# Kernel optimization log

Measured on AMD Instinct MI355X. Metric: run time of the kernel, lower is better.

The kernel has to match this reference:

```python
import jax, jax.numpy as jnp
import numpy as np

HID = 128
N_NODES = 50000
N_EDGES = 800000
N_GRAPHS = 64
N_LAYERS = 2
BN_EPS = 1e-5


def setup_inputs() -> dict:
    key = jax.random.key(0)
    ks = jax.random.split(key, 12)
    x_idx = jax.random.randint(ks[0], (N_NODES,), 0, 19)
    edge_index = jax.random.randint(ks[1], (2, N_EDGES), 0, N_NODES)
    edge_attr = jax.random.randint(ks[2], (N_EDGES,), 0, 4)
    batch = jnp.sort(jax.random.randint(ks[3], (N_NODES,), 0, N_GRAPHS))
    s = 1.0 / np.sqrt(HID)
    node_emb = jax.random.normal(ks[4], (19, HID), jnp.float32)
    edge_emb = jax.random.normal(ks[5], (4, HID), jnp.float32)
    # stacked per-layer GINE MLP params: Linear->ReLU->Linear->ReLU->BN
    W1 = jax.random.uniform(ks[6], (N_LAYERS, HID, HID), jnp.float32, -s, s)
    b1 = jnp.zeros((N_LAYERS, HID), jnp.float32)
    W2 = jax.random.uniform(ks[7], (N_LAYERS, HID, HID), jnp.float32, -s, s)
    b2 = jnp.zeros((N_LAYERS, HID), jnp.float32)
    bn_g = jnp.ones((N_LAYERS, HID), jnp.float32)
    bn_b = jnp.zeros((N_LAYERS, HID), jnp.float32)
    return {"x_idx": x_idx, "edge_index": edge_index, "edge_attr": edge_attr,
            "batch": batch, "node_emb": node_emb, "edge_emb": edge_emb,
            "W1": W1, "b1": b1, "W2": W2, "b2": b2, "bn_g": bn_g, "bn_b": bn_b}


def _gine_layer(x, e_feat, src, dst, W1, b1, W2, b2, g, beta):
    # GINEConv (eps=0): nn(x + sum_{j->i} relu(x_j + e_ji))
    msg = jax.nn.relu(x[src] + e_feat)                       # [E, H] gather
    aggr = jax.ops.segment_sum(msg, dst, num_segments=x.shape[0])  # scatter-add
    h = x + aggr
    h = jax.nn.relu(h @ W1 + b1)
    h = jax.nn.relu(h @ W2 + b2)
    mu = h.mean(0)
    var = h.var(0)
    return g * (h - mu) * jax.lax.rsqrt(var + BN_EPS) + beta  # training-mode BN


def reference(x_idx, edge_index, edge_attr, batch, node_emb, edge_emb,
              W1, b1, W2, b2, bn_g, bn_b):
    x = node_emb[x_idx]                 # [N, H]
    e_feat = edge_emb[edge_attr]        # [E, H] (encoded once, shared by layers)
    src, dst = edge_index[0], edge_index[1]
    for l in range(N_LAYERS):
        x = _gine_layer(x, e_feat, src, dst, W1[l], b1[l], W2[l], b2[l], bn_g[l], bn_b[l])
    pooled = jax.ops.segment_sum(x, batch, num_segments=N_GRAPHS)  # global_add_pool
    return pooled
```

## Files before the change

kernel.cpp:

```cpp
#include <hip/hip_runtime.h>
#include <hip/hip_bf16.h>

#define HID 128
#define NNODES 50000
#define NEDGES 800000
#define NGRAPHS 64
#define BN_EPS 1e-5f
#define CAP 64

typedef __attribute__((ext_vector_type(8))) short short8;
typedef __attribute__((ext_vector_type(4))) float f32x4;

static __device__ __forceinline__ unsigned short f2bf(float v) {
  __hip_bfloat16 b = __float2bfloat16(v);
  return *reinterpret_cast<unsigned short*>(&b);
}
static __device__ __forceinline__ float bf2f(unsigned short u) {
  return __uint_as_float(((unsigned)u) << 16);
}
static __device__ __forceinline__ float lo16f(unsigned u) {
  return __uint_as_float(u << 16);
}
static __device__ __forceinline__ float hi16f(unsigned u) {
  return __uint_as_float(u & 0xFFFF0000u);
}

static __device__ __forceinline__ unsigned packhl(float v) {
  unsigned short h = f2bf(v);
  unsigned short l = f2bf(v - bf2f(h));
  return (unsigned)h | ((unsigned)l << 16);
}
static __device__ __forceinline__ float upk(unsigned p) {
  return __uint_as_float(p << 16) + __uint_as_float(p & 0xFFFF0000u);
}
static __device__ __forceinline__ void unpack8(uint4 wa, uint4 wb,
                                               short8& hi, short8& lo) {
  union U { unsigned u[4]; short8 s; };
  U H, L;
  unsigned w[8] = {wa.x, wa.y, wa.z, wa.w, wb.x, wb.y, wb.z, wb.w};
  #pragma unroll
  for (int t = 0; t < 4; t++) {
    unsigned a = w[2 * t], b = w[2 * t + 1];
    H.u[t] = (a & 0xFFFFu) | (b << 16);
    L.u[t] = (a >> 16) | (b & 0xFFFF0000u);
  }
  hi = H.s; lo = L.s;
}

__global__ __launch_bounds__(256) void prep_kernel(
    const int* __restrict__ x_idx, const float* __restrict__ node_emb,
    const int* __restrict__ eidx, const int* __restrict__ eattr,
    int* __restrict__ cnt, int* __restrict__ eout,
    const float* __restrict__ W1, const float* __restrict__ W2,
    unsigned short* __restrict__ Wpk, unsigned* __restrict__ msgTg,
    unsigned* __restrict__ typeT, const float* __restrict__ edge_emb) {
  int i = blockIdx.x * 256 + threadIdx.x;
  int stride = gridDim.x * 256;
  for (int e = i; e < NEDGES; e += stride) {
    int s = eidx[e];
    int d = eidx[NEDGES + e];
    int ty = x_idx[s];
    int pos = atomicAdd(&cnt[d], 1);
    if (pos < CAP)
      eout[((size_t)d << 6) + pos] = s | (eattr[e] << 16) | (ty << 18);
  }
  for (int idx = i; idx < 76 * 64; idx += stride) {
    int combo = idx >> 6, c2 = (idx & 63) << 1;
    int ty = combo >> 2, at = combo & 3;
    float a0 = fmaxf(node_emb[ty * HID + c2] + edge_emb[at * HID + c2], 0.f);
    float a1 = fmaxf(node_emb[ty * HID + c2 + 1] + edge_emb[at * HID + c2 + 1], 0.f);
    msgTg[idx] = (unsigned)f2bf(a0) | ((unsigned)f2bf(a1) << 16);
  }
  for (int idx = i; idx < 19 * 64; idx += stride) {
    int ty = idx >> 6, c2 = (idx & 63) << 1;
    typeT[idx] = (unsigned)f2bf(node_emb[ty * HID + c2]) |
                 ((unsigned)f2bf(node_emb[ty * HID + c2 + 1]) << 16);
  }
  for (int idx = i; idx < 65536; idx += stride) {
    int j = idx & 7;
    int l = (idx >> 3) & 63;
    int q = (idx >> 9) & 3;
    int t = (idx >> 11) & 7;
    int m = idx >> 14;
    int k = ((l >> 4) << 3) + j + (q << 5);
    int n = (t << 4) + (l & 15);
    int layer = m >> 1;
    const float* W = (m & 1) ? W2 : W1;
    float w = W[(size_t)layer * HID * HID + k * HID + n];
    unsigned short h = f2bf(w);
    Wpk[idx] = h;
    Wpk[idx + 65536] = f2bf(w - bf2f(h));
  }
}

#define NT 32
#define LDAF 132
#define GRID_GINE ((NNODES + NT - 1) / NT)

template <bool L0>
__global__ __launch_bounds__(512, 8) void gine_mlp_kernel(
    const unsigned short* __restrict__ in_bf,
    const int* __restrict__ xidx,
    const float* __restrict__ instats,
    const float* __restrict__ gam, const float* __restrict__ bet,
    const int* __restrict__ cnt, const int* __restrict__ eout,
    const unsigned* __restrict__ msgTg, const float* __restrict__ edge_emb,
    const short8* __restrict__ Wh, const short8* __restrict__ Wl,
    const float* __restrict__ b1, const float* __restrict__ b2,
    unsigned short* __restrict__ out_bf, float* __restrict__ stats,
    const int* __restrict__ batch, float* __restrict__ gpool) {
  extern __shared__ __align__(16) char smem[];
  unsigned* hAp = (unsigned*)smem;
  float* sheL = (float*)(smem + NT * LDAF * 4);
  float* red = (float*)(smem + NT * LDAF * 4);

  const int tid = threadIdx.x;
  const int lane = tid & 63;
  const int wave = tid >> 6;
  const int base = blockIdx.x * NT;

  float scl_lo = 1.0f, scl_hi = 1.0f, sh_lo = 0.0f, sh_hi = 0.0f;

  if constexpr (!L0) {
    if (tid < 4 * HID) {
      int c = tid & 127;
      float mu = instats[c] * (1.0f / NNODES);
      float var = instats[HID + c] * (1.0f / NNODES) - mu * mu;
      float s = gam[c] * rsqrtf(var + BN_EPS);
      float shc = bet[c] - mu * s;
      sheL[tid] = shc + edge_emb[tid];
    }
    {
      int c0 = lane << 1;
      float mu0 = instats[c0] * (1.0f / NNODES);
      float var0 = instats[HID + c0] * (1.0f / NNODES) - mu0 * mu0;
      scl_lo = gam[c0] * rsqrtf(var0 + BN_EPS);
      sh_lo = bet[c0] - mu0 * scl_lo;
      float mu1 = instats[c0 + 1] * (1.0f / NNODES);
      float var1 = instats[HID + c0 + 1] * (1.0f / NNODES) - mu1 * mu1;
      scl_hi = gam[c0 + 1] * rsqrtf(var1 + BN_EPS);
      sh_hi = bet[c0 + 1] - mu1 * scl_hi;
    }
    __syncthreads();
  }

  {
    const unsigned* in4 = (const unsigned*)in_bf;
    int node0 = base + wave * 4;
    float acc0[4], acc1[4];
    #pragma unroll
    for (int i = 0; i < 4; i++) { acc0[i] = 0.0f; acc1[i] = 0.0f; }

    int dg4[4], epw4[4];
    unsigned sv4[4];
    #pragma unroll
    for (int i = 0; i < 4; i++) {
      int node = node0 + i;
      bool v = node < NNODES;
      dg4[i] = v ? __builtin_amdgcn_readfirstlane(min(cnt[node], CAP)) : 0;
      epw4[i] = v ? eout[(node << 6) + lane] : 0;
      int srow;
      if constexpr (L0)
        srow = v ? __builtin_amdgcn_readfirstlane(xidx[node]) : 0;
      else
        srow = node;
      sv4[i] = v ? in4[(srow << 6) + lane] : 0u;
    }

#define GL_ISSUE(SB, X, A)                                      \
    {                                                           \
      _Pragma("unroll")                                         \
      for (int jj = 0; jj < 8; jj++) {                          \
        if ((SB) + jj < dg) {                                   \
          int w = __builtin_amdgcn_readlane(epw, (SB) + jj);    \
          A[jj] = (w >> 16) & 3;                                \
          X[jj] = in4[((w & 0xFFFF) << 6) + lane];              \
        }                                                       \
      }                                                         \
    }
#define GL_CONS(SB, X, A)                                       \
    {                                                           \
      _Pragma("unroll")                                         \
      for (int jj = 0; jj < 8; jj++) {                          \
        if ((SB) + jj < dg) {                                   \
          float2 e2 = *(const float2*)&sheL[(A[jj] << 7) + (lane << 1)]; \
          acc0[i] += fmaxf(fmaf(lo16f(X[jj]), scl_lo, e2.x), 0.0f); \
          acc1[i] += fmaxf(fmaf(hi16f(X[jj]), scl_hi, e2.y), 0.0f); \
        }                                                       \
      }                                                         \
    }
#define GT_ISSUE(SB, M)                                         \
    {                                                           \
      _Pragma("unroll")                                         \
      for (int jj = 0; jj < 8; jj++) {                          \
        if ((SB) + jj < dg) {                                   \
          int w = __builtin_amdgcn_readlane(epw, (SB) + jj);    \
          M[jj] = msgTg[(((w >> 16) & 127) << 6) + lane];       \
        }                                                       \
      }                                                         \
    }
#define GT_CONS(SB, M)                                          \
    {                                                           \
      _Pragma("unroll")                                         \
      for (int jj = 0; jj < 8; jj++) {                          \
        if ((SB) + jj < dg) {                                   \
          acc0[i] += lo16f(M[jj]);                              \
          acc1[i] += hi16f(M[jj]);                              \
        }                                                       \
      }                                                         \
    }

    #pragma unroll
    for (int i = 0; i < 4; i++) {
      int node = node0 + i;
      if (node >= NNODES) continue;
      int dg = dg4[i];
      int epw = epw4[i];
      if constexpr (L0) {
        acc0[i] = lo16f(sv4[i]);
        acc1[i] = hi16f(sv4[i]);
      } else {
        acc0[i] = fmaf(lo16f(sv4[i]), scl_lo, sh_lo);
        acc1[i] = fmaf(hi16f(sv4[i]), scl_hi, sh_hi);
      }
      if (dg > 0) {
        if constexpr (L0) {
          unsigned M0[8], M1[8];
          GT_ISSUE(0, M0);
          int s = 0;
          for (;;) {
            if (s * 8 + 8 < dg) GT_ISSUE(s * 8 + 8, M1);
            GT_CONS(s * 8, M0);
            s++;
            if (s * 8 >= dg) break;
            if (s * 8 + 8 < dg) GT_ISSUE(s * 8 + 8, M0);
            GT_CONS(s * 8, M1);
            s++;
            if (s * 8 >= dg) break;
          }
        } else {
          unsigned X0[8], X1[8];
          int A0[8], A1[8];
          GL_ISSUE(0, X0, A0);
          int s = 0;
          for (;;) {
            if (s * 8 + 8 < dg) GL_ISSUE(s * 8 + 8, X1, A1);
            GL_CONS(s * 8, X0, A0);
            s++;
            if (s * 8 >= dg) break;
            if (s * 8 + 8 < dg) GL_ISSUE(s * 8 + 8, X0, A0);
            GL_CONS(s * 8, X1, A1);
            s++;
            if (s * 8 >= dg) break;
          }
        }
      }
    }
#undef GL_ISSUE
#undef GL_CONS
#undef GT_ISSUE
#undef GT_CONS

    #pragma unroll
    for (int i = 0; i < 4; i++) {
      int nrow = wave * 4 + i;
      hAp[nrow * LDAF + (lane << 1)] = packhl(acc0[i]);
      hAp[nrow * LDAF + (lane << 1) + 1] = packhl(acc1[i]);
    }
  }
  __syncthreads();

  const int col = lane & 15;
  const int quad = lane >> 4;
  const int rbase = quad * 4;
  const int ch0 = wave * 16 + col;
  const int aoff = quad * 8;

  {
    f32x4 a0 = {0.f, 0.f, 0.f, 0.f}, a1 = a0;
    #pragma unroll
    for (int q = 0; q < 4; q++) {
      int f0 = wave * 256 + q * 64 + lane;
      short8 b0h = Wh[f0], b0l = Wl[f0];
      const unsigned* r0 = &hAp[col * LDAF + q * 32 + aoff];
      const unsigned* r1 = &hAp[(16 + col) * LDAF + q * 32 + aoff];
      short8 a0h, a0l, a1h, a1l;
      unpack8(*(const uint4*)r0, *(const uint4*)(r0 + 4), a0h, a0l);
      unpack8(*(const uint4*)r1, *(const uint4*)(r1 + 4), a1h, a1l);
      a0 = __builtin_amdgcn_mfma_f32_16x16x32_bf16(a0h, b0h, a0, 0, 0, 0);
      a0 = __builtin_amdgcn_mfma_f32_16x16x32_bf16(a0l, b0h, a0, 0, 0, 0);
      a0 = __builtin_amdgcn_mfma_f32_16x16x32_bf16(a0h, b0l, a0, 0, 0, 0);
      a1 = __builtin_amdgcn_mfma_f32_16x16x32_bf16(a1h, b0h, a1, 0, 0, 0);
      a1 = __builtin_amdgcn_mfma_f32_16x16x32_bf16(a1l, b0h, a1, 0, 0, 0);
      a1 = __builtin_amdgcn_mfma_f32_16x16x32_bf16(a1h, b0l, a1, 0, 0, 0);
    }
    __syncthreads();
    float bb0 = b1[ch0];
    #pragma unroll
    for (int r = 0; r < 4; r++) {
      hAp[(rbase + r) * LDAF + ch0] = packhl(fmaxf(a0[r] + bb0, 0.0f));
      hAp[(16 + rbase + r) * LDAF + ch0] = packhl(fmaxf(a1[r] + bb0, 0.0f));
    }
  }
  __syncthreads();

  {
    f32x4 a0 = {0.f, 0.f, 0.f, 0.f}, a1 = a0;
    #pragma unroll
    for (int q = 0; q < 4; q++) {
      int f0 = 2048 + wave * 256 + q * 64 + lane;
      short8 b0h = Wh[f0], b0l = Wl[f0];
      const unsigned* r0 = &hAp[col * LDAF + q * 32 + aoff];
      const unsigned* r1 = &hAp[(16 + col) * LDAF + q * 32 + aoff];
      short8 a0h, a0l, a1h, a1l;
      unpack8(*(const uint4*)r0, *(const uint4*)(r0 + 4), a0h, a0l);
      unpack8(*(const uint4*)r1, *(const uint4*)(r1 + 4), a1h, a1l);
      a0 = __builtin_amdgcn_mfma_f32_16x16x32_bf16(a0h, b0h, a0, 0, 0, 0);
      a0 = __builtin_amdgcn_mfma_f32_16x16x32_bf16(a0l, b0h, a0, 0, 0, 0);
      a0 = __builtin_amdgcn_mfma_f32_16x16x32_bf16(a0h, b0l, a0, 0, 0, 0);
      a1 = __builtin_amdgcn_mfma_f32_16x16x32_bf16(a1h, b0h, a1, 0, 0, 0);
      a1 = __builtin_amdgcn_mfma_f32_16x16x32_bf16(a1l, b0h, a1, 0, 0, 0);
      a1 = __builtin_amdgcn_mfma_f32_16x16x32_bf16(a1h, b0l, a1, 0, 0, 0);
    }
    __syncthreads();
    float bb0 = b2[ch0];
    #pragma unroll
    for (int r = 0; r < 4; r++) {
      hAp[(rbase + r) * LDAF + ch0] = packhl(fmaxf(a0[r] + bb0, 0.0f));
      hAp[(16 + rbase + r) * LDAF + ch0] = packhl(fmaxf(a1[r] + bb0, 0.0f));
    }
  }
  __syncthreads();

  float lsum = 0.0f, lsq = 0.0f;
  if (tid < 256) {
    const int c = tid & 127;
    const int yy = tid >> 7;
    if (out_bf) {
      #pragma unroll 4
      for (int i = 0; i < 16; i++) {
        int n = yy * 16 + i;
        int node = base + n;
        if (node < NNODES) {
          unsigned p = hAp[n * LDAF + c];
          out_bf[node * HID + c] = (unsigned short)(p & 0xFFFF);
          float v = upk(p);
          lsum += v;
          lsq += v * v;
        }
      }
    } else {
      int curg = -1;
      float pacc = 0.0f;
      for (int i = 0; i < 16; i++) {
        int n = yy * 16 + i;
        int node = base + n;
        if (node < NNODES) {
          float v = upk(hAp[n * LDAF + c]);
          lsum += v;
          lsq += v * v;
          int bg = batch[node];
          if (bg != curg) {
            if (curg >= 0) unsafeAtomicAdd(&gpool[curg * HID + c], pacc);
            curg = bg;
            pacc = 0.0f;
          }
          pacc += v;
        }
      }
      if (curg >= 0) unsafeAtomicAdd(&gpool[curg * HID + c], pacc);
    }
    if (tid >= 128) {
      red[tid - 128] = lsum;
      red[tid] = lsq;
    }
  }
  __syncthreads();
  if (tid < 128) {
    lsum += red[tid];
    lsq += red[128 + tid];
    unsafeAtomicAdd(&stats[tid], lsum);
    unsafeAtomicAdd(&stats[HID + tid], lsq);
  }
}

__device__ __forceinline__ int lbound(const int* __restrict__ arr, int n,
                                      int key) {
  int lo = 0, hi = n;
  while (lo < hi) {
    int mid = (lo + hi) >> 1;
    if (arr[mid] < key) lo = mid + 1; else hi = mid;
  }
  return lo;
}

__global__ __launch_bounds__(128) void finish_kernel(
    const float* __restrict__ gpool, const float* __restrict__ stats,
    const float* __restrict__ gam, const float* __restrict__ bet,
    const int* __restrict__ batch, float* __restrict__ out) {
  __shared__ int cnt_s;
  int g = blockIdx.x, c = threadIdx.x;
  if (c == 0)
    cnt_s = lbound(batch, NNODES, g + 1) - lbound(batch, NNODES, g);
  __syncthreads();
  float mu = stats[c] * (1.0f / NNODES);
  float var = stats[HID + c] * (1.0f / NNODES) - mu * mu;
  float scl = gam[c] * rsqrtf(var + BN_EPS);
  float sh = bet[c] - mu * scl;
  out[g * HID + c] = fmaf(gpool[g * HID + c], scl, (float)cnt_s * sh);
}

extern "C" void kernel_launch(void* const* d_in, const int* in_sizes, int n_in,
                              void* d_out, int out_size, void* d_ws, size_t ws_size,
                              hipStream_t stream) {
  const int* x_idx = (const int*)d_in[0];
  const int* eidx = (const int*)d_in[1];
  const int* eattr = (const int*)d_in[2];
  const int* batch = (const int*)d_in[3];
  const float* node_emb = (const float*)d_in[4];
  const float* edge_emb = (const float*)d_in[5];
  const float* W1 = (const float*)d_in[6];
  const float* b1 = (const float*)d_in[7];
  const float* W2 = (const float*)d_in[8];
  const float* b2 = (const float*)d_in[9];
  const float* bn_g = (const float*)d_in[10];
  const float* bn_b = (const float*)d_in[11];
  float* out = (float*)d_out;

  const size_t nfeat = (size_t)NNODES * HID;
  unsigned short* h2bf = (unsigned short*)d_ws;
  float* stats0 = (float*)(h2bf + nfeat);
  float* stats1 = stats0 + 2 * HID;
  float* gpool = stats1 + 2 * HID;
  int* cnt = (int*)(gpool + NGRAPHS * HID);
  int* eout = cnt + NNODES;
  unsigned short* Wpk = (unsigned short*)(eout + (size_t)NNODES * CAP);
  unsigned* msgTg = (unsigned*)(Wpk + 131072);
  unsigned* typeT = msgTg + 76 * 64;
  size_t needed = (size_t)((char*)(typeT + 19 * 64) - (char*)d_ws);
  if (ws_size < needed) return;

  hipMemsetAsync(stats0, 0, (4 * HID + NGRAPHS * HID + NNODES) * sizeof(int),
                 stream);

  prep_kernel<<<1024, 256, 0, stream>>>(x_idx, node_emb, eidx, eattr, cnt,
                                        eout, W1, W2, Wpk, msgTg, typeT,
                                        edge_emb);

  const short8* Wfh = (const short8*)Wpk;
  const short8* Wfl = Wfh + 8192;
  const size_t smemsz = (size_t)NT * LDAF * 4 + 4 * HID * 4;
  gine_mlp_kernel<true><<<GRID_GINE, 512, smemsz, stream>>>(
      (const unsigned short*)typeT, x_idx, nullptr, nullptr, nullptr, cnt,
      eout, msgTg, edge_emb, Wfh + 0 * 2048, Wfl + 0 * 2048, b1, b2, h2bf,
      stats0, nullptr, nullptr);
  gine_mlp_kernel<false><<<GRID_GINE, 512, smemsz, stream>>>(
      h2bf, nullptr, stats0, bn_g, bn_b, cnt, eout, msgTg, edge_emb,
      Wfh + 2 * 2048, Wfl + 2 * 2048, b1 + HID, b2 + HID, nullptr, stats1,
      batch, gpool);
  finish_kernel<<<NGRAPHS, 128, 0, stream>>>(gpool, stats1, bn_g + HID,
                                             bn_b + HID, batch, out);
}
```

Before: 257.7 us.

## Make GINE MLP kernel persistent with atomic tile counter scheduling

The GINE layer kernels now launch a fixed grid of 1024 blocks that repeatedly grab 32-node tiles through a global atomic counter, where before there was one block per tile. BN scale/shift setup and the edge-embedding table are computed once per block instead of per tile, and the reduction scratch moves to its own shared-memory region so it no longer aliases that table. The prep kernel grid also grows from 1024 to 3125 blocks. The aim is to cut block launch overhead, amortise per-block setup and balance uneven degree work, at the cost of an atomic and extra barriers per tile.

```diff
diff --git a/kernel.cpp b/kernel.cpp
--- a/kernel.cpp
+++ b/kernel.cpp
@@ -95,7 +95,8 @@
 
 #define NT 32
 #define LDAF 132
-#define GRID_GINE ((NNODES + NT - 1) / NT)
+#define NTILES ((NNODES + NT - 1) / NT)
+#define GRID_GINE 1024
 
 template <bool L0>
 __global__ __launch_bounds__(512, 8) void gine_mlp_kernel(
@@ -108,16 +109,17 @@
     const short8* __restrict__ Wh, const short8* __restrict__ Wl,
     const float* __restrict__ b1, const float* __restrict__ b2,
     unsigned short* __restrict__ out_bf, float* __restrict__ stats,
-    const int* __restrict__ batch, float* __restrict__ gpool) {
+    const int* __restrict__ batch, float* __restrict__ gpool,
+    int* __restrict__ tilectr) {
   extern __shared__ __align__(16) char smem[];
   unsigned* hAp = (unsigned*)smem;
   float* sheL = (float*)(smem + NT * LDAF * 4);
-  float* red = (float*)(smem + NT * LDAF * 4);
+  float* red = (float*)(smem + NT * LDAF * 4 + 4 * HID * 4);
+  __shared__ int tile_s;
 
   const int tid = threadIdx.x;
   const int lane = tid & 63;
   const int wave = tid >> 6;
-  const int base = blockIdx.x * NT;
 
   float scl_lo = 1.0f, scl_hi = 1.0f, sh_lo = 0.0f, sh_hi = 0.0f;
 
@@ -141,246 +143,254 @@
       scl_hi = gam[c0 + 1] * rsqrtf(var1 + BN_EPS);
       sh_hi = bet[c0 + 1] - mu1 * scl_hi;
     }
-    __syncthreads();
-  }
-
-  {
-    const unsigned* in4 = (const unsigned*)in_bf;
-    int node0 = base + wave * 4;
-    float acc0[4], acc1[4];
-    #pragma unroll
-    for (int i = 0; i < 4; i++) { acc0[i] = 0.0f; acc1[i] = 0.0f; }
-
-    int dg4[4], epw4[4];
-    unsigned sv4[4];
-    #pragma unroll
-    for (int i = 0; i < 4; i++) {
-      int node = node0 + i;
-      bool v = node < NNODES;
-      dg4[i] = v ? __builtin_amdgcn_readfirstlane(min(cnt[node], CAP)) : 0;
-      epw4[i] = v ? eout[(node << 6) + lane] : 0;
-      int srow;
-      if constexpr (L0)
-        srow = v ? __builtin_amdgcn_readfirstlane(xidx[node]) : 0;
-      else
-        srow = node;
-      sv4[i] = v ? in4[(srow << 6) + lane] : 0u;
-    }
+  }
+
+  for (;;) {
+    if (tid == 0) tile_s = atomicAdd(tilectr, 1);
+    __syncthreads();
+    const int tile = tile_s;
+    if (tile >= NTILES) break;
+    const int base = tile * NT;
+
+    {
+      const unsigned* in4 = (const unsigned*)in_bf;
+      int node0 = base + wave * 4;
+      float acc0[4], acc1[4];
+      #pragma unroll
+      for (int i = 0; i < 4; i++) { acc0[i] = 0.0f; acc1[i] = 0.0f; }
+
+      int dg4[4], epw4[4];
+      unsigned sv4[4];
+      #pragma unroll
+      for (int i = 0; i < 4; i++) {
+        int node = node0 + i;
+        bool v = node < NNODES;
+        dg4[i] = v ? __builtin_amdgcn_readfirstlane(min(cnt[node], CAP)) : 0;
+        epw4[i] = v ? eout[(node << 6) + lane] : 0;
+        int srow;
+        if constexpr (L0)
+          srow = v ? __builtin_amdgcn_readfirstlane(xidx[node]) : 0;
+        else
+          srow = node;
+        sv4[i] = v ? in4[(srow << 6) + lane] : 0u;
+      }
 
 #define GL_ISSUE(SB, X, A)                                      \
-    {                                                           \
-      _Pragma("unroll")                                         \
-      for (int jj = 0; jj < 8; jj++) {                          \
-        if ((SB) + jj < dg) {                                   \
-          int w = __builtin_amdgcn_readlane(epw, (SB) + jj);    \
-          A[jj] = (w >> 16) & 3;                                \
-          X[jj] = in4[((w & 0xFFFF) << 6) + lane];              \
+      {                                                         \
+        _Pragma("unroll")                                       \
+        for (int jj = 0; jj < 8; jj++) {                        \
+          if ((SB) + jj < dg) {                                 \
+            int w = __builtin_amdgcn_readlane(epw, (SB) + jj);  \
+            A[jj] = (w >> 16) & 3;                              \
+            X[jj] = in4[((w & 0xFFFF) << 6) + lane];            \
+          }                                                     \
         }                                                       \
-      }                                                         \
-    }
+      }
 #define GL_CONS(SB, X, A)                                       \
-    {                                                           \
-      _Pragma("unroll")                                         \
-      for (int jj = 0; jj < 8; jj++) {                          \
-        if ((SB) + jj < dg) {                                   \
-          float2 e2 = *(const float2*)&sheL[(A[jj] << 7) + (lane << 1)]; \
-          acc0[i] += fmaxf(fmaf(lo16f(X[jj]), scl_lo, e2.x), 0.0f); \
-          acc1[i] += fmaxf(fmaf(hi16f(X[jj]), scl_hi, e2.y), 0.0f); \
+      {                                                         \
+        _Pragma("unroll")                                       \
+        for (int jj = 0; jj < 8; jj++) {                        \
+          if ((SB) + jj < dg) {                                 \
+            float2 e2 = *(const float2*)&sheL[(A[jj] << 7) + (lane << 1)]; \
+            acc0[i] += fmaxf(fmaf(lo16f(X[jj]), scl_lo, e2.x), 0.0f); \
+            acc1[i] += fmaxf(fmaf(hi16f(X[jj]), scl_hi, e2.y), 0.0f); \
+          }                                                     \
         }                                                       \
-      }                                                         \
-    }
+      }
 #define GT_ISSUE(SB, M)                                         \
-    {                                                           \
-      _Pragma("unroll")                                         \
-      for (int jj = 0; jj < 8; jj++) {                          \
-        if ((SB) + jj < dg) {                                   \
-          int w = __builtin_amdgcn_readlane(epw, (SB) + jj);    \
-          M[jj] = msgTg[(((w >> 16) & 127) << 6) + lane];       \
+      {                                                         \
+        _Pragma("unroll")                                       \
+        for (int jj = 0; jj < 8; jj++) {                        \
+          if ((SB) + jj < dg) {                                 \
+            int w = __builtin_amdgcn_readlane(epw, (SB) + jj);  \
+            M[jj] = msgTg[(((w >> 16) & 127) << 6) + lane];     \
+          }                                                     \
         }                                                       \
-      }                                                         \
-    }
+      }
 #define GT_CONS(SB, M)                                          \
-    {                                                           \
-      _Pragma("unroll")                                         \
-      for (int jj = 0; jj < 8; jj++) {                          \
-        if ((SB) + jj < dg) {                                   \
-          acc0[i] += lo16f(M[jj]);                              \
-          acc1[i] += hi16f(M[jj]);                              \
+      {                                                         \
+        _Pragma("unroll")                                       \
+        for (int jj = 0; jj < 8; jj++) {                        \
+          if ((SB) + jj < dg) {                                 \
+            acc0[i] += lo16f(M[jj]);                            \
+            acc1[i] += hi16f(M[jj]);                            \
+          }                                                     \
         }                                                       \
-      }                                                         \
-    }
-
-    #pragma unroll
-    for (int i = 0; i < 4; i++) {
-      int node = node0 + i;
-      if (node >= NNODES) continue;
-      int dg = dg4[i];
-      int epw = epw4[i];
-      if constexpr (L0) {
-        acc0[i] = lo16f(sv4[i]);
-        acc1[i] = hi16f(sv4[i]);
-      } else {
-        acc0[i] = fmaf(lo16f(sv4[i]), scl_lo, sh_lo);
-        acc1[i] = fmaf(hi16f(sv4[i]), scl_hi, sh_hi);
-      }
-      if (dg > 0) {
+      }
+
+      #pragma unroll
+      for (int i = 0; i < 4; i++) {
+        int node = node0 + i;
+        if (node >= NNODES) continue;
+        int dg = dg4[i];
+        int epw = epw4[i];
         if constexpr (L0) {
-          unsigned M0[8], M1[8];
-          GT_ISSUE(0, M0);
-          int s = 0;
-          for (;;) {
-            if (s * 8 + 8 < dg) GT_ISSUE(s * 8 + 8, M1);
-            GT_CONS(s * 8, M0);
-            s++;
-            if (s * 8 >= dg) break;
-            if (s * 8 + 8 < dg) GT_ISSUE(s * 8 + 8, M0);
-            GT_CONS(s * 8, M1);
-            s++;
-            if (s * 8 >= dg) break;
-          }
+          acc0[i] = lo16f(sv4[i]);
+          acc1[i] = hi16f(sv4[i]);
         } else {
-          unsigned X0[8], X1[8];
-          int A0[8], A1[8];
-          GL_ISSUE(0, X0, A0);
-          int s = 0;
-          for (;;) {
-            if (s * 8 + 8 < dg) GL_ISSUE(s * 8 + 8, X1, A1);
-            GL_CONS(s * 8, X0, A0);
-            s++;
-            if (s * 8 >= dg) break;
-            if (s * 8 + 8 < dg) GL_ISSUE(s * 8 + 8, X0, A0);
-            GL_CONS(s * 8, X1, A1);
-            s++;
-            if (s * 8 >= dg) break;
+          acc0[i] = fmaf(lo16f(sv4[i]), scl_lo, sh_lo);
+          acc1[i] = fmaf(hi16f(sv4[i]), scl_hi, sh_hi);
+        }
+        if (dg > 0) {
+          if constexpr (L0) {
+            unsigned M0[8], M1[8];
+            GT_ISSUE(0, M0);
+            int s = 0;
+            for (;;) {
+              if (s * 8 + 8 < dg) GT_ISSUE(s * 8 + 8, M1);
+              GT_CONS(s * 8, M0);
+              s++;
+              if (s * 8 >= dg) break;
+              if (s * 8 + 8 < dg) GT_ISSUE(s * 8 + 8, M0);
+              GT_CONS(s * 8, M1);
+              s++;
+              if (s * 8 >= dg) break;
+            }
+          } else {
+            unsigned X0[8], X1[8];
+            int A0[8], A1[8];
+            GL_ISSUE(0, X0, A0);
+            int s = 0;
+            for (;;) {
+              if (s * 8 + 8 < dg) GL_ISSUE(s * 8 + 8, X1, A1);
+              GL_CONS(s * 8, X0, A0);
+              s++;
+              if (s * 8 >= dg) break;
+              if (s * 8 + 8 < dg) GL_ISSUE(s * 8 + 8, X0, A0);
+              GL_CONS(s * 8, X1, A1);
+              s++;
+              if (s * 8 >= dg) break;
+            }
           }
         }
       }
-    }
 #undef GL_ISSUE
 #undef GL_CONS
 #undef GT_ISSUE
 #undef GT_CONS
 
-    #pragma unroll
-    for (int i = 0; i < 4; i++) {
-      int nrow = wave * 4 + i;
-      hAp[nrow * LDAF + (lane << 1)] = packhl(acc0[i]);
-      hAp[nrow * LDAF + (lane << 1) + 1] = packhl(acc1[i]);
-    }
-  }
-  __syncthreads();
-
-  const int col = lane & 15;
-  const int quad = lane >> 4;
-  const int rbase = quad * 4;
-  const int ch0 = wave * 16 + col;
-  const int aoff = quad * 8;
-
-  {
-    f32x4 a0 = {0.f, 0.f, 0.f, 0.f}, a1 = a0;
-    #pragma unroll
-    for (int q = 0; q < 4; q++) {
-      int f0 = wave * 256 + q * 64 + lane;
-      short8 b0h = Wh[f0], b0l = Wl[f0];
-      const unsigned* r0 = &hAp[col * LDAF + q * 32 + aoff];
-      const unsigned* r1 = &hAp[(16 + col) * LDAF + q * 32 + aoff];
-      short8 a0h, a0l, a1h, a1l;
-      unpack8(*(const uint4*)r0, *(const uint4*)(r0 + 4), a0h, a0l);
-      unpack8(*(const uint4*)r1, *(const uint4*)(r1 + 4), a1h, a1l);
-      a0 = __builtin_amdgcn_mfma_f32_16x16x32_bf16(a0h, b0h, a0, 0, 0, 0);
-      a0 = __builtin_amdgcn_mfma_f32_16x16x32_bf16(a0l, b0h, a0, 0, 0, 0);
-      a0 = __builtin_amdgcn_mfma_f32_16x16x32_bf16(a0h, b0l, a0, 0, 0, 0);
-      a1 = __builtin_amdgcn_mfma_f32_16x16x32_bf16(a1h, b0h, a1, 0, 0, 0);
-      a1 = __builtin_amdgcn_mfma_f32_16x16x32_bf16(a1l, b0h, a1, 0, 0, 0);
-      a1 = __builtin_amdgcn_mfma_f32_16x16x32_bf16(a1h, b0l, a1, 0, 0, 0);
-    }
-    __syncthreads();
-    float bb0 = b1[ch0];
-    #pragma unroll
-    for (int r = 0; r < 4; r++) {
-      hAp[(rbase + r) * LDAF + ch0] = packhl(fmaxf(a0[r] + bb0, 0.0f));
-      hAp[(16 + rbase + r) * LDAF + ch0] = packhl(fmaxf(a1[r] + bb0, 0.0f));
-    }
-  }
-  __syncthreads();
-
-  {
-    f32x4 a0 = {0.f, 0.f, 0.f, 0.f}, a1 = a0;
-    #pragma unroll
-    for (int q = 0; q < 4; q++) {
-      int f0 = 2048 + wave * 256 + q * 64 + lane;
-      short8 b0h = Wh[f0], b0l = Wl[f0];
-      const unsigned* r0 = &hAp[col * LDAF + q * 32 + aoff];
-      const unsigned* r1 = &hAp[(16 + col) * LDAF + q * 32 + aoff];
-      short8 a0h, a0l, a1h, a1l;
-      unpack8(*(const uint4*)r0, *(const uint4*)(r0 + 4), a0h, a0l);
-      unpack8(*(const uint4*)r1, *(const uint4*)(r1 + 4), a1h, a1l);
-      a0 = __builtin_amdgcn_mfma_f32_16x16x32_bf16(a0h, b0h, a0, 0, 0, 0);
-      a0 = __builtin_amdgcn_mfma_f32_16x16x32_bf16(a0l, b0h, a0, 0, 0, 0);
-      a0 = __builtin_amdgcn_mfma_f32_16x16x32_bf16(a0h, b0l, a0, 0, 0, 0);
-      a1 = __builtin_amdgcn_mfma_f32_16x16x32_bf16(a1h, b0h, a1, 0, 0, 0);
-      a1 = __builtin_amdgcn_mfma_f32_16x16x32_bf16(a1l, b0h, a1, 0, 0, 0);
-      a1 = __builtin_amdgcn_mfma_f32_16x16x32_bf16(a1h, b0l, a1, 0, 0, 0);
-    }
-    __syncthreads();
-    float bb0 = b2[ch0];
-    #pragma unroll
-    for (int r = 0; r < 4; r++) {
-      hAp[(rbase + r) * LDAF + ch0] = packhl(fmaxf(a0[r] + bb0, 0.0f));
-      hAp[(16 + rbase + r) * LDAF + ch0] = packhl(fmaxf(a1[r] + bb0, 0.0f));
-    }
-  }
-  __syncthreads();
-
-  float lsum = 0.0f, lsq = 0.0f;
-  if (tid < 256) {
-    const int c = tid & 127;
-    const int yy = tid >> 7;
-    if (out_bf) {
-      #pragma unroll 4
-      for (int i = 0; i < 16; i++) {
-        int n = yy * 16 + i;
-        int node = base + n;
-        if (node < NNODES) {
-          unsigned p = hAp[n * LDAF + c];
-          out_bf[node * HID + c] = (unsigned short)(p & 0xFFFF);
-          float v = upk(p);
-          lsum += v;
-          lsq += v * v;
+      #pragma unroll
+      for (int i = 0; i < 4; i++) {
+        int nrow = wave * 4 + i;
+        hAp[nrow * LDAF + (lane << 1)] = packhl(acc0[i]);
+        hAp[nrow * LDAF + (lane << 1) + 1] = packhl(acc1[i]);
+      }
+    }
+    __syncthreads();
+
+    const int col = lane & 15;
+    const int quad = lane >> 4;
+    const int rbase = quad * 4;
+    const int ch0 = wave * 16 + col;
+    const int aoff = quad * 8;
+
+    {
+      f32x4 a0 = {0.f, 0.f, 0.f, 0.f}, a1 = a0;
+      #pragma unroll
+      for (int q = 0; q < 4; q++) {
+        int f0 = wave * 256 + q * 64 + lane;
+        short8 b0h = Wh[f0], b0l = Wl[f0];
+        const unsigned* r0 = &hAp[col * LDAF + q * 32 + aoff];
+        const unsigned* r1 = &hAp[(16 + col) * LDAF + q * 32 + aoff];
+        short8 a0h, a0l, a1h, a1l;
+        unpack8(*(const uint4*)r0, *(const uint4*)(r0 + 4), a0h, a0l);
+        unpack8(*(const uint4*)r1, *(const uint4*)(r1 + 4), a1h, a1l);
+        a0 = __builtin_amdgcn_mfma_f32_16x16x32_bf16(a0h, b0h, a0, 0, 0, 0);
+        a0 = __builtin_amdgcn_mfma_f32_16x16x32_bf16(a0l, b0h, a0, 0, 0, 0);
+        a0 = __builtin_amdgcn_mfma_f32_16x16x32_bf16(a0h, b0l, a0, 0, 0, 0);
+        a1 = __builtin_amdgcn_mfma_f32_16x16x32_bf16(a1h, b0h, a1, 0, 0, 0);
+        a1 = __builtin_amdgcn_mfma_f32_16x16x32_bf16(a1l, b0h, a1, 0, 0, 0);
+        a1 = __builtin_amdgcn_mfma_f32_16x16x32_bf16(a1h, b0l, a1, 0, 0, 0);
+      }
+      __syncthreads();
+      float bb0 = b1[ch0];
+      #pragma unroll
+      for (int r = 0; r < 4; r++) {
+        hAp[(rbase + r) * LDAF + ch0] = packhl(fmaxf(a0[r] + bb0, 0.0f));
+        hAp[(16 + rbase + r) * LDAF + ch0] = packhl(fmaxf(a1[r] + bb0, 0.0f));
+      }
+    }
+    __syncthreads();
+
+    {
+      f32x4 a0 = {0.f, 0.f, 0.f, 0.f}, a1 = a0;
+      #pragma unroll
+      for (int q = 0; q < 4; q++) {
+        int f0 = 2048 + wave * 256 + q * 64 + lane;
+        short8 b0h = Wh[f0], b0l = Wl[f0];
+        const unsigned* r0 = &hAp[col * LDAF + q * 32 + aoff];
+        const unsigned* r1 = &hAp[(16 + col) * LDAF + q * 32 + aoff];
+        short8 a0h, a0l, a1h, a1l;
+        unpack8(*(const uint4*)r0, *(const uint4*)(r0 + 4), a0h, a0l);
+        unpack8(*(const uint4*)r1, *(const uint4*)(r1 + 4), a1h, a1l);
+        a0 = __builtin_amdgcn_mfma_f32_16x16x32_bf16(a0h, b0h, a0, 0, 0, 0);
+        a0 = __builtin_amdgcn_mfma_f32_16x16x32_bf16(a0l, b0h, a0, 0, 0, 0);
+        a0 = __builtin_amdgcn_mfma_f32_16x16x32_bf16(a0h, b0l, a0, 0, 0, 0);
+        a1 = __builtin_amdgcn_mfma_f32_16x16x32_bf16(a1h, b0h, a1, 0, 0, 0);
+        a1 = __builtin_amdgcn_mfma_f32_16x16x32_bf16(a1l, b0h, a1, 0, 0, 0);
+        a1 = __builtin_amdgcn_mfma_f32_16x16x32_bf16(a1h, b0l, a1, 0, 0, 0);
+      }
+      __syncthreads();
+      float bb0 = b2[ch0];
+      #pragma unroll
+      for (int r = 0; r < 4; r++) {
+        hAp[(rbase + r) * LDAF + ch0] = packhl(fmaxf(a0[r] + bb0, 0.0f));
+        hAp[(16 + rbase + r) * LDAF + ch0] = packhl(fmaxf(a1[r] + bb0, 0.0f));
+      }
+    }
+    __syncthreads();
+
+    float lsum = 0.0f, lsq = 0.0f;
+    if (tid < 256) {
+      const int c = tid & 127;
+      const int yy = tid >> 7;
+      if (out_bf) {
+        #pragma unroll 4
+        for (int i = 0; i < 16; i++) {
+          int n = yy * 16 + i;
+          int node = base + n;
+          if (node < NNODES) {
+            unsigned p = hAp[n * LDAF + c];
+            out_bf[node * HID + c] = (unsigned short)(p & 0xFFFF);
+            float v = upk(p);
+            lsum += v;
+            lsq += v * v;
+          }
         }
-      }
-    } else {
-      int curg = -1;
-      float pacc = 0.0f;
-      for (int i = 0; i < 16; i++) {
-        int n = yy * 16 + i;
-        int node = base + n;
-        if (node < NNODES) {
-          float v = upk(hAp[n * LDAF + c]);
-          lsum += v;
-          lsq += v * v;
-          int bg = batch[node];
-          if (bg != curg) {
-            if (curg >= 0) unsafeAtomicAdd(&gpool[curg * HID + c], pacc);
-            curg = bg;
-            pacc = 0.0f;
+      } else {
+        int curg = -1;
+        float pacc = 0.0f;
+        for (int i = 0; i < 16; i++) {
+          int n = yy * 16 + i;
+          int node = base + n;
+          if (node < NNODES) {
+            float v = upk(hAp[n * LDAF + c]);
+            lsum += v;
+            lsq += v * v;
+            int bg = batch[node];
+            if (bg != curg) {
+              if (curg >= 0) unsafeAtomicAdd(&gpool[curg * HID + c], pacc);
+              curg = bg;
+              pacc = 0.0f;
+            }
+            pacc += v;
           }
-          pacc += v;
         }
-      }
-      if (curg >= 0) unsafeAtomicAdd(&gpool[curg * HID + c], pacc);
-    }
-    if (tid >= 128) {
-      red[tid - 128] = lsum;
-      red[tid] = lsq;
-    }
-  }
-  __syncthreads();
-  if (tid < 128) {
-    lsum += red[tid];
-    lsq += red[128 + tid];
-    unsafeAtomicAdd(&stats[tid], lsum);
-    unsafeAtomicAdd(&stats[HID + tid], lsq);
+        if (curg >= 0) unsafeAtomicAdd(&gpool[curg * HID + c], pacc);
+      }
+      if (tid >= 128) {
+        red[tid - 128] = lsum;
+        red[tid] = lsq;
+      }
+    }
+    __syncthreads();
+    if (tid < 128) {
+      lsum += red[tid];
+      lsq += red[128 + tid];
+      unsafeAtomicAdd(&stats[tid], lsum);
+      unsafeAtomicAdd(&stats[HID + tid], lsq);
+    }
+    __syncthreads();
   }
 }
 
@@ -433,31 +443,32 @@
   float* stats1 = stats0 + 2 * HID;
   float* gpool = stats1 + 2 * HID;
   int* cnt = (int*)(gpool + NGRAPHS * HID);
-  int* eout = cnt + NNODES;
+  int* tilec = cnt + NNODES;
+  int* eout = tilec + 2;
   unsigned short* Wpk = (unsigned short*)(eout + (size_t)NNODES * CAP);
   unsigned* msgTg = (unsigned*)(Wpk + 131072);
   unsigned* typeT = msgTg + 76 * 64;
   size_t needed = (size_t)((char*)(typeT + 19 * 64) - (char*)d_ws);
   if (ws_size < needed) return;
 
-  hipMemsetAsync(stats0, 0, (4 * HID + NGRAPHS * HID + NNODES) * sizeof(int),
-                 stream);
-
-  prep_kernel<<<1024, 256, 0, stream>>>(x_idx, node_emb, eidx, eattr, cnt,
+  hipMemsetAsync(stats0, 0,
+                 (4 * HID + NGRAPHS * HID + NNODES + 2) * sizeof(int), stream);
+
+  prep_kernel<<<3125, 256, 0, stream>>>(x_idx, node_emb, eidx, eattr, cnt,
                                         eout, W1, W2, Wpk, msgTg, typeT,
                                         edge_emb);
 
   const short8* Wfh = (const short8*)Wpk;
   const short8* Wfl = Wfh + 8192;
-  const size_t smemsz = (size_t)NT * LDAF * 4 + 4 * HID * 4;
+  const size_t smemsz = (size_t)NT * LDAF * 4 + 4 * HID * 4 + 256 * 4;
   gine_mlp_kernel<true><<<GRID_GINE, 512, smemsz, stream>>>(
       (const unsigned short*)typeT, x_idx, nullptr, nullptr, nullptr, cnt,
       eout, msgTg, edge_emb, Wfh + 0 * 2048, Wfl + 0 * 2048, b1, b2, h2bf,
-      stats0, nullptr, nullptr);
+      stats0, nullptr, nullptr, tilec + 0);
   gine_mlp_kernel<false><<<GRID_GINE, 512, smemsz, stream>>>(
       h2bf, nullptr, stats0, bn_g, bn_b, cnt, eout, msgTg, edge_emb,
       Wfh + 2 * 2048, Wfl + 2 * 2048, b1 + HID, b2 + HID, nullptr, stats1,
-      batch, gpool);
+      batch, gpool, tilec + 1);
   finish_kernel<<<NGRAPHS, 128, 0, stream>>>(gpool, stats1, bn_g + HID,
                                              bn_b + HID, batch, out);
 }
```

Result: slower. 346.3 us (+34.4%).
